# Kernel tuning notes

Measured on AMD Instinct MI355X. Metric: run time of the kernel, lower is better.

Reference implementation:

```python
import jax, jax.numpy as jnp
import numpy as np

M = 28            # mask head resolution (mask_logit[i] is MxM)
NUM_CLASSES = 80  # max value of cls_idx (mask_image channel count)


def setup_inputs() -> dict:
    key = jax.random.key(0)
    k1, k2, k3, k4, k5, k6, k7 = jax.random.split(key, 7)
    N, H, W = 100, 800, 800
    cx = jax.random.uniform(k1, (N,), minval=0.0, maxval=float(W - 1))
    cy = jax.random.uniform(k2, (N,), minval=0.0, maxval=float(H - 1))
    bw = jax.random.uniform(k3, (N,), minval=20.0, maxval=300.0)
    bh = jax.random.uniform(k4, (N,), minval=20.0, maxval=300.0)
    mask_rois = jnp.stack([cx - bw / 2, cy - bh / 2, cx + bw / 2, cy + bh / 2], axis=1).astype(jnp.float32)
    cls_prob = jax.random.uniform(k5, (N,), dtype=jnp.float32)
    mask_prob = jax.random.normal(k6, (N, M, M), dtype=jnp.float32)
    cls_idx = jax.random.randint(k7, (N,), 1, NUM_CLASSES + 1, dtype=jnp.int32)
    return {"mask_rois": mask_rois, "cls_prob": cls_prob, "mask_prob": mask_prob,
            "cls_idx": cls_idx, "im_h": H, "im_w": W}


def _paste(logit, box, H, W):
    """Bilinear-paste an MxM logit into the full HxW image (== cv2.resize to (w,h)
    then placing at the box, evaluated directly on image pixel coords)."""
    x0, y0, x1, y1 = box[0], box[1], box[2], box[3]  # int32
    w = jnp.maximum(x1 - x0 + 1, 1).astype(jnp.float32)
    h = jnp.maximum(y1 - y0 + 1, 1).astype(jnp.float32)
    xs = jnp.arange(W, dtype=jnp.float32)
    ys = jnp.arange(H, dtype=jnp.float32)
    # cv2 bilinear mapping: src = (dst + 0.5) * (M / size) - 0.5, clamped at borders
    sx = jnp.clip((xs - x0.astype(jnp.float32) + 0.5) * (M / w) - 0.5, 0.0, M - 1.0)
    sy = jnp.clip((ys - y0.astype(jnp.float32) + 0.5) * (M / h) - 0.5, 0.0, M - 1.0)
    ix0 = jnp.floor(sx).astype(jnp.int32); ix1 = jnp.minimum(ix0 + 1, M - 1); fx = sx - ix0
    iy0 = jnp.floor(sy).astype(jnp.int32); iy1 = jnp.minimum(iy0 + 1, M - 1); fy = sy - iy0
    v00 = logit[iy0[:, None], ix0[None, :]]
    v01 = logit[iy0[:, None], ix1[None, :]]
    v10 = logit[iy1[:, None], ix0[None, :]]
    v11 = logit[iy1[:, None], ix1[None, :]]
    val = ((1 - fy)[:, None] * ((1 - fx)[None, :] * v00 + fx[None, :] * v01)
           + fy[:, None] * ((1 - fx)[None, :] * v10 + fx[None, :] * v11))
    xi = jnp.arange(W, dtype=jnp.int32)
    yi = jnp.arange(H, dtype=jnp.int32)
    inside_x = (xi >= jnp.maximum(x0, 0)) & (xi < jnp.minimum(x1 + 1, W))
    inside_y = (yi >= jnp.maximum(y0, 0)) & (yi < jnp.minimum(y1 + 1, H))
    inside = inside_y[:, None] & inside_x[None, :]
    return jnp.where(inside, val, 0.0), inside


def _forward(mask_rois, cls_prob, mask_prob, cls_idx, H, W, thr):
    N = mask_prob.shape[0]
    order = jnp.argsort(-cls_prob)                       # sort by score, descending
    boxes = mask_rois[order].astype(jnp.int32)
    logits = mask_prob[order]
    cls = cls_idx[order].astype(jnp.int32) - 1           # 0-based class ids
    pasted, inside = jax.vmap(lambda l, b: _paste(l, b, H, W))(logits, boxes)  # [N,H,W]

    def step(mask_image, xs):
        logit, ins, c = xs
        mask = (logit > 0) & ins                          # thresholded, in-image crop mask
        prev = mask_image[c]
        msum = jnp.sum(mask).astype(jnp.float32)
        ovl = jnp.sum(mask & prev).astype(jnp.float32)    # overlap with accumulated class mask
        keep = (msum > 0) & (ovl <= thr * msum)           # skip if ratio > threshold
        mask_image = mask_image.at[c].set(prev | (mask & keep))
        return mask_image, keep

    mask_image0 = jnp.zeros((NUM_CLASSES, H, W), dtype=bool)
    _, keep = jax.lax.scan(step, mask_image0, (pasted, inside, cls))

    # compact kept masks to the front (frame_id order); dropped boxes go to slot N (discarded)
    pos = jnp.where(keep, jnp.cumsum(keep.astype(jnp.int32)) - 1, N)
    energy = jnp.where(inside & keep[:, None, None], pasted, 0.0)
    full = jnp.zeros((N + 1, H, W), pasted.dtype).at[pos].set(energy)
    mask_energy = full[:N][None]                          # [1, N, H, W], kept masks first
    keep_inds = jnp.full((N + 1,), -1, jnp.int32).at[pos].set(
        jnp.where(keep, order.astype(jnp.int32), -1))[:N]
    return keep_inds, mask_energy


def reference(mask_rois, cls_prob, mask_prob, cls_idx, im_h, im_w):
    return _forward(mask_rois, cls_prob, mask_prob, cls_idx, int(im_h), int(im_w), 0.3)
```

## Files before the change

### kernel.cpp

```cpp
#include <hip/hip_runtime.h>

#define NINST 100
#define MLOG 28
#define IMG 800
#define LOGSZ (MLOG * MLOG)

#define OFF_ORDER 0
#define OFF_CLS   100
#define OFF_BOX   200
#define OFF_MSUM  600
#define OFF_SLOT  800
#define OFF_NK    900
#define OFF_FLAG  904
#define OFF_MASK  1024
#define ROWW      12
#define MSTRIDE   (ROWW * 304)
#define PAIR_CAP  512
#define SLOTSZ    (IMG * IMG)
#define SUBB      20
#define ROWSPB    (IMG / SUBB)
#define MEGAGRID  (1 + NINST * SUBB)

__global__ __launch_bounds__(256) void k_raster(const float* __restrict__ mask_prob,
                                                const float* __restrict__ cls_prob,
                                                const float* __restrict__ rois,
                                                const int* __restrict__ cls_idx,
                                                int* __restrict__ ws) {
    int b = blockIdx.x, tid = threadIdx.x;
    __shared__ float s_p[NINST];
    __shared__ int s_order[NINST];
    __shared__ float lg[LOGSZ];
    __shared__ int red[256];
    if (tid < NINST) s_p[tid] = cls_prob[tid];
    __syncthreads();
    if (tid < NINST) {
        float p = s_p[tid];
        int r = 0;
        for (int j = 0; j < NINST; j++) {
            float q = s_p[j];
            r += (q > p) || (q == p && j < tid);
        }
        s_order[r] = tid;
    }
    __syncthreads();
    int n = b;
    int orig = s_order[n];
    int x0 = (int)rois[4 * orig], y0 = (int)rois[4 * orig + 1];
    int x1 = (int)rois[4 * orig + 2], y1 = (int)rois[4 * orig + 3];
    if (b == 0) {
        if (tid == 0) ws[OFF_FLAG] = 0;
        if (tid < NINST) {
            int o = s_order[tid];
            ws[OFF_ORDER + tid] = o;
            ws[OFF_CLS + tid] = cls_idx[o] - 1;
#pragma unroll
            for (int k = 0; k < 4; k++)
                ws[OFF_BOX + 4 * tid + k] = (int)rois[4 * o + k];
        }
    }
    for (int i = tid; i < LOGSZ; i += 256) lg[i] = mask_prob[orig * LOGSZ + i];
    __syncthreads();
    int xs = max(x0, 0), xe = min(x1 + 1, IMG);
    int ys = max(y0, 0), ye = min(y1 + 1, IMG);
    int wx0 = xs >> 5, nw = ((xe + 31) >> 5) - wx0, nrows = ye - ys;
    float wf = fmaxf((float)(x1 - x0 + 1), 1.f), hf = fmaxf((float)(y1 - y0 + 1), 1.f);
    float rx = 28.f / wf, ry = 28.f / hf;
    unsigned* mb = (unsigned*)(ws + OFF_MASK) + n * MSTRIDE;
    int total = nrows * nw, cnt = 0;
    for (int t = tid; t < total; t += 256) {
        int row = t / nw, wc = t - row * nw;
        int y = ys + row;
        float sy = ((float)y - (float)y0 + 0.5f) * ry - 0.5f;
        sy = fminf(fmaxf(sy, 0.f), 27.f);
        int iy0 = (int)sy, iy1 = min(iy0 + 1, 27);
        float fy = sy - (float)iy0;
        const float* r0 = lg + iy0 * MLOG;
        const float* r1 = lg + iy1 * MLOG;
        unsigned bits = 0u;
        int xbase = (wx0 + wc) << 5;
        int j0 = max(xs - xbase, 0), j1 = min(xe - xbase, 32);
        for (int j = j0; j < j1; j++) {
            int xx = xbase + j;
            float sx = ((float)xx - (float)x0 + 0.5f) * rx - 0.5f;
            sx = fminf(fmaxf(sx, 0.f), 27.f);
            int ix0 = (int)sx, ix1 = min(ix0 + 1, 27);
            float fx = sx - (float)ix0;
            float val = (1.f - fy) * ((1.f - fx) * r0[ix0] + fx * r0[ix1]) +
                        fy * ((1.f - fx) * r1[ix0] + fx * r1[ix1]);
            bits |= (val > 0.f) ? (1u << j) : 0u;
        }
        mb[row * ROWW + wc] = bits;
        cnt += __popc(bits);
    }
    red[tid] = cnt;
    __syncthreads();
    for (int s = 128; s; s >>= 1) {
        if (tid < s) red[tid] += red[tid + s];
        __syncthreads();
    }
    if (tid == 0) ws[OFF_MSUM + n] = red[0];
}

__global__ __launch_bounds__(256, 8) void k_mega(const float* __restrict__ mask_prob,
                                                 int* __restrict__ ws,
                                                 float* __restrict__ out) {
    int b = blockIdx.x, tid = threadIdx.x;
    const unsigned* maskbase = (const unsigned*)(ws + OFF_MASK);
    if (b > 0) {
        int s = (b - 1) / SUBB, sub = (b - 1) - s * SUBB;
        int r0 = sub * ROWSPB;
        float4* z = (float4*)(out + NINST + (size_t)s * SLOTSZ + (size_t)r0 * IMG);
        for (int t = tid; t < (ROWSPB * IMG / 4); t += 256)
            z[t] = make_float4(0.f, 0.f, 0.f, 0.f);
        __syncthreads();
        if (tid == 0) {
            while (__hip_atomic_load(ws + OFF_FLAG, __ATOMIC_RELAXED,
                                     __HIP_MEMORY_SCOPE_AGENT) == 0)
                __builtin_amdgcn_s_sleep(16);
            __builtin_amdgcn_fence(__ATOMIC_ACQUIRE, "agent");
        }
        __syncthreads();
        int nk = ws[OFF_NK];
        if (s >= nk) return;
        int n = ws[OFF_SLOT + s];
        const int* box = ws + OFF_BOX + 4 * n;
        int x0 = box[0], y0 = box[1], x1 = box[2], y1 = box[3];
        int xs = max(x0, 0), xe = min(x1 + 1, IMG);
        int ys = max(y0, 0), ye = min(y1 + 1, IMG);
        int ya = max(ys, r0), yb = min(ye, r0 + ROWSPB);
        if (ya >= yb) return;
        __shared__ float lg[LOGSZ];
        int orig = ws[OFF_ORDER + n];
        for (int i = tid; i < LOGSZ; i += 256) lg[i] = mask_prob[orig * LOGSZ + i];
        __syncthreads();
        int xa = xs & ~3;
        int w4 = (xe - xa + 3) >> 2;
        int total = (yb - ya) * w4;
        float rx = 28.f / fmaxf((float)(x1 - x0 + 1), 1.f);
        float ry = 28.f / fmaxf((float)(y1 - y0 + 1), 1.f);
        float* sbase = out + NINST + (size_t)s * SLOTSZ;
        for (int t = tid; t < total; t += 256) {
            int row = t / w4, c4 = t - row * w4;
            int y = ya + row, xb = xa + (c4 << 2);
            float sy = ((float)y - (float)y0 + 0.5f) * ry - 0.5f;
            sy = fminf(fmaxf(sy, 0.f), 27.f);
            int iy0 = (int)sy, iy1 = min(iy0 + 1, 27);
            float fy = sy - (float)iy0;
            const float* rr0 = lg + iy0 * MLOG;
            const float* rr1 = lg + iy1 * MLOG;
            float vq[4];
#pragma unroll
            for (int j = 0; j < 4; j++) {
                int xx = xb + j;
                float val = 0.f;
                if (xx >= xs && xx < xe) {
                    float sx = ((float)xx - (float)x0 + 0.5f) * rx - 0.5f;
                    sx = fminf(fmaxf(sx, 0.f), 27.f);
                    int ix0 = (int)sx, ix1 = min(ix0 + 1, 27);
                    float fx = sx - (float)ix0;
                    val = (1.f - fy) * ((1.f - fx) * rr0[ix0] + fx * rr0[ix1]) +
                          fy * ((1.f - fx) * rr1[ix0] + fx * rr1[ix1]);
                }
                vq[j] = val;
            }
            *(float4*)(sbase + (size_t)y * IMG + xb) = make_float4(vq[0], vq[1], vq[2], vq[3]);
        }
        return;
    }
    __shared__ int s_cls[NINST], s_msum[NINST], s_box[4 * NINST];
    __shared__ int s_wi[PAIR_CAP], s_wj[PAIR_CAP], s_po[PAIR_CAP];
    __shared__ int s_nw;
    __shared__ int s_cand[32];
    for (int i = tid; i < NINST; i += 256) {
        s_cls[i] = ws[OFF_CLS + i];
        s_msum[i] = ws[OFF_MSUM + i];
    }
    for (int i = tid; i < 4 * NINST; i += 256) s_box[i] = ws[OFF_BOX + i];
    if (tid == 0) s_nw = 0;
    __syncthreads();
    for (int c = tid; c < NINST * NINST; c += 256) {
        int i = c / NINST, j = c - i * NINST;
        if (i >= j) continue;
        if (s_cls[i] != s_cls[j]) continue;
        if (s_msum[i] == 0 || s_msum[j] == 0) continue;
        int ixs = max(s_box[4 * i], 0), ixe = min(s_box[4 * i + 2] + 1, IMG);
        int iys = max(s_box[4 * i + 1], 0), iye = min(s_box[4 * i + 3] + 1, IMG);
        int jxs = max(s_box[4 * j], 0), jxe = min(s_box[4 * j + 2] + 1, IMG);
        int jys = max(s_box[4 * j + 1], 0), jye = min(s_box[4 * j + 3] + 1, IMG);
        if (!(ixs < jxe && jxs < ixe && iys < jye && jys < iye)) continue;
        int k = atomicAdd(&s_nw, 1);
        if (k < PAIR_CAP) { s_wi[k] = i; s_wj[k] = j; }
    }
    __syncthreads();
    int nw = min(s_nw, PAIR_CAP);
    int wid = tid >> 6, lane = tid & 63;
    for (int k = wid; k < nw; k += 4) {
        int i = s_wi[k], j = s_wj[k];
        int ixs = max(s_box[4 * i], 0), ixe = min(s_box[4 * i + 2] + 1, IMG);
        int iys = max(s_box[4 * i + 1], 0), iye = min(s_box[4 * i + 3] + 1, IMG);
        int jxs = max(s_box[4 * j], 0), jxe = min(s_box[4 * j + 2] + 1, IMG);
        int jys = max(s_box[4 * j + 1], 0);
        int iwx0 = ixs >> 5, jwx0 = jxs >> 5;
        int wlo = max(iwx0, jwx0);
        int whi = min((ixe + 31) >> 5, (jxe + 31) >> 5);
        int rlo = max(iys, jys);
        int rhi = min(iye, min(s_box[4 * j + 3] + 1, IMG));
        int nwrd = whi - wlo, nrows = rhi - rlo;
        const unsigned* mi = maskbase + i * MSTRIDE;
        const unsigned* mj = maskbase + j * MSTRIDE;
        int total = nrows * nwrd, cnt = 0;
        for (int t = lane; t < total; t += 64) {
            int row = t / nwrd, wc = t - row * nwrd;
            int y = rlo + row, w = wlo + wc;
            unsigned a = mi[(y - iys) * ROWW + (w - iwx0)];
            unsigned bb = mj[(y - jys) * ROWW + (w - jwx0)];
            cnt += __popc(a & bb);
        }
        for (int off = 32; off; off >>= 1) cnt += __shfl_down(cnt, off);
        if (lane == 0) s_po[k] = cnt;
    }
    __syncthreads();
    if (tid >= 64) return;
    unsigned long long k0 = 0, k1 = 0;
    for (int n = 0; n < NINST; n++) {
        int msum = s_msum[n];
        int lsum = 0, lmax = 0, lcnt = 0;
        for (int q = lane; q < nw; q += 64) {
            if (s_wj[q] == n) {
                int pi = s_wi[q];
                bool kb = (pi < 64) ? ((k0 >> pi) & 1ull) : ((k1 >> (pi - 64)) & 1ull);
                if (kb) { int o = s_po[q]; lsum += o; lmax = max(lmax, o); lcnt++; }
            }
        }
        for (int off = 32; off; off >>= 1) {
            lsum += __shfl_xor(lsum, off);
            lmax = max(lmax, __shfl_xor(lmax, off));
            lcnt += __shfl_xor(lcnt, off);
        }
        float thr = 0.3f * (float)msum;
        int keep;
        if (lcnt == 0 || (float)lsum <= thr) keep = (msum > 0);
        else if ((float)lmax > thr) keep = 0;
        else {
            int nc = 0;
            for (int q0 = 0; q0 < nw; q0 += 64) {
                int q = q0 + lane;
                bool p = false; int piv = 0;
                if (q < nw && s_wj[q] == n) {
                    piv = s_wi[q];
                    p = (piv < 64) ? ((k0 >> piv) & 1ull) : ((k1 >> (piv - 64)) & 1ull);
                }
                unsigned long long m = __ballot(p);
                int pos = nc + __popcll(m & ((1ull << lane) - 1ull));
                if (p && pos < 32) s_cand[pos] = piv;
                nc += __popcll(m);
            }
            nc = min(nc, 32);
            asm volatile("s_waitcnt lgkmcnt(0)" ::: "memory");
            __builtin_amdgcn_sched_barrier(0);
            int nxs = max(s_box[4 * n], 0), nxe = min(s_box[4 * n + 2] + 1, IMG);
            int nys = max(s_box[4 * n + 1], 0), nye = min(s_box[4 * n + 3] + 1, IMG);
            int wx0 = nxs >> 5, nwrd = ((nxe + 31) >> 5) - wx0, nrows = nye - nys;
            const unsigned* mn = maskbase + n * MSTRIDE;
            int total = nrows * nwrd, ovl = 0;
            for (int t2 = lane; t2 < total; t2 += 64) {
                int row = t2 / nwrd, wc = t2 - row * nwrd;
                unsigned bits = mn[row * ROWW + wc];
                if (!bits) continue;
                int y = nys + row, wa = wx0 + wc;
                unsigned img = 0;
                for (int k = 0; k < nc; k++) {
                    int m2 = s_cand[k];
                    int mys = max(s_box[4 * m2 + 1], 0), mye = min(s_box[4 * m2 + 3] + 1, IMG);
                    int mxs = max(s_box[4 * m2], 0), mxe = min(s_box[4 * m2 + 2] + 1, IMG);
                    int mwx0 = mxs >> 5, mnw = ((mxe + 31) >> 5) - mwx0;
                    int rr = y - mys, cc = wa - mwx0;
                    if (rr >= 0 && rr < (mye - mys) && cc >= 0 && cc < mnw)
                        img |= maskbase[m2 * MSTRIDE + rr * ROWW + cc];
                }
                ovl += __popc(bits & img);
            }
            for (int off = 32; off; off >>= 1) ovl += __shfl_xor(ovl, off);
            keep = (msum > 0) && ((float)ovl <= thr);
        }
        if (keep) { if (n < 64) k0 |= 1ull << n; else k1 |= 1ull << (n - 64); }
    }
    if (lane == 0) {
        int nk = 0;
        for (int n = 0; n < NINST; n++) {
            bool kb = (n < 64) ? ((k0 >> n) & 1ull) : ((k1 >> (n - 64)) & 1ull);
            if (kb) {
                ws[OFF_SLOT + nk] = n;
                out[nk] = (float)ws[OFF_ORDER + n];
                nk++;
            }
        }
        ws[OFF_NK] = nk;
        for (int s2 = nk; s2 < NINST; s2++) out[s2] = -1.f;
        __builtin_amdgcn_fence(__ATOMIC_RELEASE, "agent");
        __hip_atomic_store(ws + OFF_FLAG, 1, __ATOMIC_RELAXED,
                           __HIP_MEMORY_SCOPE_AGENT);
    }
}

extern "C" void kernel_launch(void* const* d_in, const int* in_sizes, int n_in,
                              void* d_out, int out_size, void* d_ws, size_t ws_size,
                              hipStream_t stream) {
    const float* rois      = (const float*)d_in[0];
    const float* cls_prob  = (const float*)d_in[1];
    const float* mask_prob = (const float*)d_in[2];
    const int*   cls_idx   = (const int*)d_in[3];
    int* ws = (int*)d_ws;
    float* out = (float*)d_out;

    k_raster<<<dim3(NINST), dim3(256), 0, stream>>>(mask_prob, cls_prob, rois, cls_idx, ws);
    k_mega<<<dim3(MEGAGRID), dim3(256), 0, stream>>>(mask_prob, ws, out);
}
```

Measured before the change: 376.9 us.

## Split fused mega kernel into zero+scan kernel and separate box paste kernel

Replaces the single mega kernel, which spin-waited on a global flag before pasting, with two launches. The first launch zeroes the whole output with a grid-stride loop while block 0 runs the greedy scan. The second launch pastes each kept box in a 2D grid over slots and tiles. This removes the in-kernel flag spin and the per-slot row-band blocks that often had no work, at the cost of an extra launch boundary that serializes the paste after zeroing finishes.

```diff
diff --git a/kernel.cpp b/kernel.cpp
--- a/kernel.cpp
+++ b/kernel.cpp
@@ -11,15 +11,12 @@
 #define OFF_MSUM  600
 #define OFF_SLOT  800
 #define OFF_NK    900
-#define OFF_FLAG  904
 #define OFF_MASK  1024
 #define ROWW      12
 #define MSTRIDE   (ROWW * 304)
 #define PAIR_CAP  512
-#define SLOTSZ    (IMG * IMG)
-#define SUBB      20
-#define ROWSPB    (IMG / SUBB)
-#define MEGAGRID  (1 + NINST * SUBB)
+#define ZTOT      (IMG * IMG * NINST / 4)
+#define ZBLKS     4096
 
 __global__ __launch_bounds__(256) void k_raster(const float* __restrict__ mask_prob,
                                                 const float* __restrict__ cls_prob,
@@ -48,7 +45,6 @@
     int x0 = (int)rois[4 * orig], y0 = (int)rois[4 * orig + 1];
     int x1 = (int)rois[4 * orig + 2], y1 = (int)rois[4 * orig + 3];
     if (b == 0) {
-        if (tid == 0) ws[OFF_FLAG] = 0;
         if (tid < NINST) {
             int o = s_order[tid];
             ws[OFF_ORDER + tid] = o;
@@ -101,72 +97,15 @@
     if (tid == 0) ws[OFF_MSUM + n] = red[0];
 }
 
-__global__ __launch_bounds__(256, 8) void k_mega(const float* __restrict__ mask_prob,
-                                                 int* __restrict__ ws,
-                                                 float* __restrict__ out) {
+__global__ __launch_bounds__(256) void k_scan_zero(int* __restrict__ ws, float* __restrict__ out) {
     int b = blockIdx.x, tid = threadIdx.x;
+    if (b > 0) {
+        float4* z = (float4*)(out + NINST);
+        for (size_t pi = (size_t)(b - 1) * 256 + tid; pi < (size_t)ZTOT; pi += (size_t)ZBLKS * 256)
+            z[pi] = make_float4(0.f, 0.f, 0.f, 0.f);
+        return;
+    }
     const unsigned* maskbase = (const unsigned*)(ws + OFF_MASK);
-    if (b > 0) {
-        int s = (b - 1) / SUBB, sub = (b - 1) - s * SUBB;
-        int r0 = sub * ROWSPB;
-        float4* z = (float4*)(out + NINST + (size_t)s * SLOTSZ + (size_t)r0 * IMG);
-        for (int t = tid; t < (ROWSPB * IMG / 4); t += 256)
-            z[t] = make_float4(0.f, 0.f, 0.f, 0.f);
-        __syncthreads();
-        if (tid == 0) {
-            while (__hip_atomic_load(ws + OFF_FLAG, __ATOMIC_RELAXED,
-                                     __HIP_MEMORY_SCOPE_AGENT) == 0)
-                __builtin_amdgcn_s_sleep(16);
-            __builtin_amdgcn_fence(__ATOMIC_ACQUIRE, "agent");
-        }
-        __syncthreads();
-        int nk = ws[OFF_NK];
-        if (s >= nk) return;
-        int n = ws[OFF_SLOT + s];
-        const int* box = ws + OFF_BOX + 4 * n;
-        int x0 = box[0], y0 = box[1], x1 = box[2], y1 = box[3];
-        int xs = max(x0, 0), xe = min(x1 + 1, IMG);
-        int ys = max(y0, 0), ye = min(y1 + 1, IMG);
-        int ya = max(ys, r0), yb = min(ye, r0 + ROWSPB);
-        if (ya >= yb) return;
-        __shared__ float lg[LOGSZ];
-        int orig = ws[OFF_ORDER + n];
-        for (int i = tid; i < LOGSZ; i += 256) lg[i] = mask_prob[orig * LOGSZ + i];
-        __syncthreads();
-        int xa = xs & ~3;
-        int w4 = (xe - xa + 3) >> 2;
-        int total = (yb - ya) * w4;
-        float rx = 28.f / fmaxf((float)(x1 - x0 + 1), 1.f);
-        float ry = 28.f / fmaxf((float)(y1 - y0 + 1), 1.f);
-        float* sbase = out + NINST + (size_t)s * SLOTSZ;
-        for (int t = tid; t < total; t += 256) {
-            int row = t / w4, c4 = t - row * w4;
-            int y = ya + row, xb = xa + (c4 << 2);
-            float sy = ((float)y - (float)y0 + 0.5f) * ry - 0.5f;
-            sy = fminf(fmaxf(sy, 0.f), 27.f);
-            int iy0 = (int)sy, iy1 = min(iy0 + 1, 27);
-            float fy = sy - (float)iy0;
-            const float* rr0 = lg + iy0 * MLOG;
-            const float* rr1 = lg + iy1 * MLOG;
-            float vq[4];
-#pragma unroll
-            for (int j = 0; j < 4; j++) {
-                int xx = xb + j;
-                float val = 0.f;
-                if (xx >= xs && xx < xe) {
-                    float sx = ((float)xx - (float)x0 + 0.5f) * rx - 0.5f;
-                    sx = fminf(fmaxf(sx, 0.f), 27.f);
-                    int ix0 = (int)sx, ix1 = min(ix0 + 1, 27);
-                    float fx = sx - (float)ix0;
-                    val = (1.f - fy) * ((1.f - fx) * rr0[ix0] + fx * rr0[ix1]) +
-                          fy * ((1.f - fx) * rr1[ix0] + fx * rr1[ix1]);
-                }
-                vq[j] = val;
-            }
-            *(float4*)(sbase + (size_t)y * IMG + xb) = make_float4(vq[0], vq[1], vq[2], vq[3]);
-        }
-        return;
-    }
     __shared__ int s_cls[NINST], s_msum[NINST], s_box[4 * NINST];
     __shared__ int s_wi[PAIR_CAP], s_wj[PAIR_CAP], s_po[PAIR_CAP];
     __shared__ int s_nw;
@@ -297,9 +236,55 @@
         }
         ws[OFF_NK] = nk;
         for (int s2 = nk; s2 < NINST; s2++) out[s2] = -1.f;
-        __builtin_amdgcn_fence(__ATOMIC_RELEASE, "agent");
-        __hip_atomic_store(ws + OFF_FLAG, 1, __ATOMIC_RELAXED,
-                           __HIP_MEMORY_SCOPE_AGENT);
+    }
+}
+
+__global__ __launch_bounds__(256) void k_box(const float* __restrict__ mask_prob,
+                                             const int* __restrict__ ws,
+                                             float* __restrict__ out) {
+    int slot = blockIdx.y, tid = threadIdx.x;
+    if (slot >= ws[OFF_NK]) return;
+    int n = ws[OFF_SLOT + slot];
+    const int* box = ws + OFF_BOX + 4 * n;
+    int x0 = box[0], y0 = box[1], x1 = box[2], y1 = box[3];
+    int xs = max(x0, 0), xe = min(x1 + 1, IMG);
+    int ys = max(y0, 0), ye = min(y1 + 1, IMG);
+    int xa = xs & ~3;
+    int w4 = (xe - xa + 3) >> 2;
+    int rows = ye - ys;
+    int total = rows * w4;
+    __shared__ float lg[LOGSZ];
+    int orig = ws[OFF_ORDER + n];
+    for (int i = tid; i < LOGSZ; i += 256) lg[i] = mask_prob[orig * LOGSZ + i];
+    __syncthreads();
+    float wf = fmaxf((float)(x1 - x0 + 1), 1.f), hf = fmaxf((float)(y1 - y0 + 1), 1.f);
+    float rx = 28.f / wf, ry = 28.f / hf;
+    float* base = out + NINST + (size_t)slot * (IMG * IMG);
+    for (int t = blockIdx.x * 256 + tid; t < total; t += gridDim.x * 256) {
+        int row = t / w4, c4 = t - row * w4;
+        int y = ys + row, xb = xa + (c4 << 2);
+        float sy = ((float)y - (float)y0 + 0.5f) * ry - 0.5f;
+        sy = fminf(fmaxf(sy, 0.f), 27.f);
+        int iy0 = (int)sy, iy1 = min(iy0 + 1, 27);
+        float fy = sy - (float)iy0;
+        const float* r0 = lg + iy0 * MLOG;
+        const float* r1 = lg + iy1 * MLOG;
+        float v[4];
+#pragma unroll
+        for (int j = 0; j < 4; j++) {
+            int xx = xb + j;
+            float val = 0.f;
+            if (xx >= xs && xx < xe) {
+                float sx = ((float)xx - (float)x0 + 0.5f) * rx - 0.5f;
+                sx = fminf(fmaxf(sx, 0.f), 27.f);
+                int ix0 = (int)sx, ix1 = min(ix0 + 1, 27);
+                float fx = sx - (float)ix0;
+                val = (1.f - fy) * ((1.f - fx) * r0[ix0] + fx * r0[ix1]) +
+                      fy * ((1.f - fx) * r1[ix0] + fx * r1[ix1]);
+            }
+            v[j] = val;
+        }
+        *(float4*)(base + (size_t)y * IMG + xb) = make_float4(v[0], v[1], v[2], v[3]);
     }
 }
 
@@ -314,5 +299,6 @@
     float* out = (float*)d_out;
 
     k_raster<<<dim3(NINST), dim3(256), 0, stream>>>(mask_prob, cls_prob, rois, cls_idx, ws);
-    k_mega<<<dim3(MEGAGRID), dim3(256), 0, stream>>>(mask_prob, ws, out);
+    k_scan_zero<<<dim3(1 + ZBLKS), dim3(256), 0, stream>>>(ws, out);
+    k_box<<<dim3(91, NINST), dim3(256), 0, stream>>>(mask_prob, ws, out);
 }
```

Measured after the change: 352.2 us. 6.6% less time.
